# Kernel tuning notes

Measured on AMD Instinct MI355X. Metric: run time of the kernel, lower is better.

Reference implementation:

```python
import jax, jax.numpy as jnp
import numpy as np

B, E, H, LEVELS, MAXN = 16, 256, 256, 12, 2
N = 2 ** LEVELS - 1  # 4095 nodes, level-order perfect binary tree
NODE_VOCAB, EDGE_VOCAB = 64, 128

PARAM_SHAPES = {
    'node_emb': (NODE_VOCAB, E), 'edge_emb': (EDGE_VOCAB, E),
    'bu_Wioux': (E, 3 * H), 'bu_bioux': (3 * H,), 'bu_Wfx': (E, H), 'bu_bfx': (H,),
    'bu_Wiouh': (MAXN * H, 3 * H), 'bu_Wfh': (MAXN, MAXN * H, H),
    'bu_eWih': (E, 4 * H), 'bu_eWhh': (H, 4 * H), 'bu_ebih': (4 * H,), 'bu_ebhh': (4 * H,),
    'td_Wioux': (E, 3 * H), 'td_bioux': (3 * H,), 'td_Wfx': (E, H), 'td_bfx': (H,),
    'td_Wiouhc': (MAXN * H, 3 * H), 'td_Wiouhp': (H, 3 * H),
    'td_Wfchild': (MAXN, (MAXN + 1) * H, H), 'td_Wfparent': ((MAXN + 1) * H, H),
    'td_eWih': (E, 4 * H), 'td_eWhh': (H, 4 * H), 'td_ebih': (4 * H,), 'td_ebhh': (4 * H,),
}
FLOAT_NAMES = list(PARAM_SHAPES)

_sig = jax.nn.sigmoid

def _lstm(x, h, c, Wih, Whh, bih, bhh):
    # torch nn.LSTMCell gate order: i, f, g, o
    g = x @ Wih + h @ Whh + bih + bhh
    i, f, gg, o = jnp.split(g, 4, axis=-1)
    c2 = _sig(f) * c + _sig(i) * jnp.tanh(gg)
    return _sig(o) * jnp.tanh(c2), c2

def _forward(p, node_ids, edge_ids):
    x_all = p['node_emb'][node_ids]  # [B,N,E]
    e_all = p['edge_emb'][edge_ids]  # [B,N,E] edge to parent
    bu_h = [None] * LEVELS
    bu_he = [None] * LEVELS
    bu_ce = [None] * LEVELS
    # ---- bottom-up n-ary TreeLSTM, level by level (deepest first) ----
    for l in range(LEVELS - 1, -1, -1):
        M = 2 ** l
        s = M - 1
        x = x_all[:, s:s + M]
        if l == LEVELS - 1:  # leaves: zero-padded children (no fc terms)
            ch_h = jnp.zeros((B, M, MAXN, H), x.dtype)
            ch_c = ch_h
        else:
            ch_h = bu_he[l + 1].reshape(B, M, MAXN, H)
            ch_c = bu_ce[l + 1].reshape(B, M, MAXN, H)
        cat = ch_h.reshape(B, M, MAXN * H)  # child_cat_h
        iou = x @ p['bu_Wioux'] + p['bu_bioux'] + cat @ p['bu_Wiouh']
        i, o, u = jnp.split(iou, 3, axis=-1)
        i, o, u = _sig(i), _sig(o), jnp.tanh(u)
        fx = x @ p['bu_Wfx'] + p['bu_bfx']
        f = _sig(fx[:, :, None, :] + jnp.einsum('bmc,kch->bmkh', cat, p['bu_Wfh']))
        c = i * u + (f * ch_c).sum(axis=2)
        h = o * jnp.tanh(c)
        bu_h[l] = h
        # edge-transition LSTMCell before passing state to parent
        he, ce = _lstm(e_all[:, s:s + M], h, c, p['bu_eWih'], p['bu_eWhh'], p['bu_ebih'], p['bu_ebhh'])
        bu_he[l] = he
        bu_ce[l] = ce
    # ---- top-down n-ary TreeLSTM (root first) ----
    td_h = [None] * LEVELS
    ph = jnp.zeros((B, 1, H), x_all.dtype)
    pc = ph
    for l in range(LEVELS):
        M = 2 ** l
        s = M - 1
        x = x_all[:, s:s + M]
        if l == LEVELS - 1:
            ch_h = jnp.zeros((B, M, MAXN, H), x.dtype)
            ch_c = ch_h
        else:
            ch_h = bu_he[l + 1].reshape(B, M, MAXN, H)
            ch_c = bu_ce[l + 1].reshape(B, M, MAXN, H)
        cat = ch_h.reshape(B, M, MAXN * H)
        iou = x @ p['td_Wioux'] + p['td_bioux'] + cat @ p['td_Wiouhc'] + ph @ p['td_Wiouhp']
        i, o, u = jnp.split(iou, 3, axis=-1)
        i, o, u = _sig(i), _sig(o), jnp.tanh(u)
        fx = x @ p['td_Wfx'] + p['td_bfx']
        pcat = jnp.concatenate([ph, cat], axis=-1)  # [B,M,(MAXN+1)H]
        f_ch = _sig(fx[:, :, None, :] + jnp.einsum('bmc,kch->bmkh', pcat, p['td_Wfchild']))
        f_par = _sig(fx + pcat @ p['td_Wfparent'])
        c = i * u + (f_ch * ch_c).sum(axis=2) + f_par * pc
        h = o * jnp.tanh(c)
        td_h[l] = h
        if l < LEVELS - 1:
            M2 = 2 * M
            s2 = 2 * M - 1
            ph_r = jnp.repeat(h, 2, axis=1)
            pc_r = jnp.repeat(c, 2, axis=1)
            ph, pc = _lstm(e_all[:, s2:s2 + M2], ph_r, pc_r, p['td_eWih'], p['td_eWhh'], p['td_ebih'], p['td_ebhh'])
    return jnp.concatenate([jnp.concatenate(bu_h, 1), jnp.concatenate(td_h, 1)], axis=-1)  # [B,N,2H]


def setup_inputs() -> dict:
    key = jax.random.key(0)
    ks = jax.random.split(key, len(PARAM_SHAPES) + 2)
    inp = {}
    for k, (name, shp) in zip(ks, PARAM_SHAPES.items()):
        inp[name] = jax.random.normal(k, shp, dtype=jnp.float32) * 0.05
    inp['node_ids'] = jax.random.randint(ks[-2], (B, N), 0, NODE_VOCAB)
    inp['edge_ids'] = jax.random.randint(ks[-1], (B, N), 0, EDGE_VOCAB)
    return inp


def reference(node_emb, edge_emb, bu_Wioux, bu_bioux, bu_Wfx, bu_bfx, bu_Wiouh, bu_Wfh,
              bu_eWih, bu_eWhh, bu_ebih, bu_ebhh, td_Wioux, td_bioux, td_Wfx, td_bfx,
              td_Wiouhc, td_Wiouhp, td_Wfchild, td_Wfparent, td_eWih, td_eWhh, td_ebih, td_ebhh,
              node_ids, edge_ids):
    floats = (node_emb, edge_emb, bu_Wioux, bu_bioux, bu_Wfx, bu_bfx, bu_Wiouh, bu_Wfh,
              bu_eWih, bu_eWhh, bu_ebih, bu_ebhh, td_Wioux, td_bioux, td_Wfx, td_bfx,
              td_Wiouhc, td_Wiouhp, td_Wfchild, td_Wfparent, td_eWih, td_eWhh, td_ebih, td_ebhh)
    return _forward(dict(zip(FLOAT_NAMES, floats)), node_ids, edge_ids)
```

## Files before the change

### kernel.cpp

```cpp
#include <hip/hip_runtime.h>
#include <math.h>

#define NB 16
#define NH 256
#define NLV 12
#define NN 4095
#define OUTW 512

typedef unsigned short u16;
typedef unsigned int u32;
typedef __attribute__((ext_vector_type(4))) float f32x4;
typedef __attribute__((ext_vector_type(8))) short bf16x8;

__device__ __forceinline__ float sigf(float x){
  return __fdividef(1.0f, 1.0f + __expf(-x));
}
__device__ __forceinline__ float tanh_fast(float x){
  return 1.0f - __fdividef(2.0f, 1.0f + __expf(2.0f * x));
}

__device__ __forceinline__ u16 f2bf(float x){
  unsigned int u = __float_as_uint(x);
  return (u16)((u + 0x7fffu + ((u >> 16) & 1u)) >> 16);
}
__device__ __forceinline__ float bf2f(u16 h){
  return __uint_as_float(((unsigned int)h) << 16);
}

__device__ __forceinline__ void gload16(const void* g, void* l){
  __builtin_amdgcn_global_load_lds(
      (const __attribute__((address_space(1))) unsigned int*)g,
      (__attribute__((address_space(3))) unsigned int*)l, 16, 0, 0);
}

template<int VAR, int NG>
__global__ __launch_bounds__(256, 2) void fused_gemm(
    int R, int logM, int s,
    const int* __restrict__ ids,
    const u16* __restrict__ emb,
    const u16* __restrict__ hsrc,
    const u16* __restrict__ hsrc2,
    const u16* __restrict__ Wth, int wstride,
    const float* __restrict__ bias,
    const float* __restrict__ cce,
    const float* __restrict__ cprev,
    float* __restrict__ c_out,
    u16* __restrict__ h_out,
    float* __restrict__ out)
{
  constexpr int K0 = 256;
  constexpr int K1 = (VAR == 0) ? 512 : 256;
  constexpr int K2 = (VAR == 2 && NG == 6) ? 512 : 0;
  constexpr int KTOT = K0 + K1 + K2;
  constexpr int NSTEP = KTOT / 64;

  __shared__ u16 As[2][128][64];
  __shared__ u16 Bs[2][NG * 32][64];

  int bx = blockIdx.x;
  if ((gridDim.x & 7) == 0){
    int q = (int)gridDim.x >> 3;
    bx = (bx & 7) * q + (bx >> 3);
  }

  int tid = threadIdx.x, lane = tid & 63, w = tid >> 6;
  int wrow = w >> 1, whh = w & 1;
  int hh0 = blockIdx.y * 32;
  int M = 1 << logM;

  int lrow8 = lane >> 3;
  int gran  = lane & 7;
  int swz = (gran ^ lrow8) * 8;

  u32 off0[4]; u32 off1[4]; u32 off2[4];
  #pragma unroll
  for (int c = 0; c < 4; ++c){
    int gr = bx * 128 + c * 32 + w * 8 + lrow8;
    if (gr > R - 1) gr = R - 1;
    int b = gr >> logM, m = gr & (M - 1);
    int j = s + m;
    off0[c] = (u32)ids[b * NN + j] * 256u + (u32)swz;
    if constexpr (VAR == 0)
      off1[c] = (u32)(b * NN + 2 * j + 1) * (u32)NH + (u32)swz;
    else if constexpr (VAR == 3)
      off1[c] = (u32)(b * (M >> 1) + (m >> 1)) * (u32)NH + (u32)swz;
    else
      off1[c] = (u32)gr * (u32)NH + (u32)swz;
    if constexpr (K2 > 0)
      off2[c] = (u32)(b * NN + 2 * j + 1) * (u32)NH + (u32)swz;
    else
      off2[c] = 0;
  }
  u32 offB = (u32)(hh0 + w * 8 + lrow8) * (u32)wstride + (u32)swz;

  auto stage = [&](int buf, int kt){
    #pragma unroll
    for (int c = 0; c < 4; ++c){
      const u16* ga;
      if (kt < K0)               ga = emb   + off0[c] + kt;
      else if (kt < K0 + K1)     ga = hsrc  + off1[c] + (kt - K0);
      else                       ga = hsrc2 + off2[c] + (kt - K0 - K1);
      gload16(ga, &As[buf][c * 32 + w * 8][0]);
    }
    #pragma unroll
    for (int g = 0; g < NG; ++g)
      gload16(Wth + offB + (u32)(g * 256) * (u32)wstride + kt,
              &Bs[buf][g * 32 + w * 8][0]);
  };

  f32x4 acc[NG][4];
  #pragma unroll
  for (int g = 0; g < NG; ++g)
    #pragma unroll
    for (int i = 0; i < 4; ++i) acc[g][i] = (f32x4)0.0f;

  stage(0, 0);
  __syncthreads();

  #pragma unroll
  for (int st = 0; st < NSTEP; ++st){
    const int cur = st & 1;
    if (st + 1 < NSTEP) stage(cur ^ 1, (st + 1) * 64);

    #pragma unroll
    for (int kc = 0; kc < 2; ++kc){
      int g2 = ((kc * 4 + (lane >> 4)) ^ (lane & 7)) * 8;
      bf16x8 a[4];
      #pragma unroll
      for (int i = 0; i < 4; ++i)
        a[i] = *(const bf16x8*)&As[cur][wrow * 64 + i * 16 + (lane & 15)][g2];
      bf16x8 bf[NG];
      #pragma unroll
      for (int g = 0; g < NG; ++g)
        bf[g] = *(const bf16x8*)&Bs[cur][g * 32 + whh * 16 + (lane & 15)][g2];
      #pragma unroll
      for (int g = 0; g < NG; ++g)
        #pragma unroll
        for (int i = 0; i < 4; ++i)
          acc[g][i] = __builtin_amdgcn_mfma_f32_16x16x32_bf16(a[i], bf[g], acc[g][i], 0, 0, 0);
    }
    __syncthreads();
  }

  int hhL = hh0 + whh * 16 + (lane & 15);
  float bb[NG];
  #pragma unroll
  for (int g = 0; g < NG; ++g) bb[g] = bias[g * 256 + hhL];

  #pragma unroll
  for (int i = 0; i < 4; ++i){
    #pragma unroll
    for (int r = 0; r < 4; ++r){
      int row = bx * 128 + wrow * 64 + i * 16 + ((lane >> 4) << 2) + r;
      if (row >= R) continue;
      int b = row >> logM, m = row & (M - 1);
      int j = s + m;
      if constexpr (VAR == 0){
        float iv = sigf(acc[0][i][r] + bb[0]);
        float ov = sigf(acc[1][i][r] + bb[1]);
        float uv = tanh_fast(acc[2][i][r] + bb[2]);
        float c = iv * uv;
        float f0 = sigf(acc[3][i][r] + bb[3]);
        float f1 = sigf(acc[4 % NG][i][r] + bb[4 % NG]);
        c += f0 * cce[((size_t)(b * NN + 2 * j + 1)) * NH + hhL]
           + f1 * cce[((size_t)(b * NN + 2 * j + 2)) * NH + hhL];
        float h = ov * tanh_fast(c);
        c_out[(size_t)row * NH + hhL] = c;
        h_out[(size_t)row * NH + hhL] = f2bf(h);
        out[((size_t)(b * NN + j)) * OUTW + hhL] = h;
      } else if constexpr (VAR == 1){
        float iv = sigf(acc[0][i][r] + bb[0]);
        float fv = sigf(acc[1][i][r] + bb[1]);
        float gg = tanh_fast(acc[2][i][r] + bb[2]);
        float ov = sigf(acc[3 % NG][i][r] + bb[3 % NG]);
        float c2 = fv * cprev[(size_t)row * NH + hhL] + iv * gg;
        float h2 = ov * tanh_fast(c2);
        size_t di = ((size_t)(b * NN + j)) * NH + hhL;
        h_out[di] = f2bf(h2);
        c_out[di] = c2;
      } else if constexpr (VAR == 2){
        float iv = sigf(acc[0][i][r] + bb[0]);
        float ov = sigf(acc[1][i][r] + bb[1]);
        float uv = tanh_fast(acc[2][i][r] + bb[2]);
        float fp = sigf(acc[3 % NG][i][r] + bb[3 % NG]);
        float c = iv * uv + fp * cprev[(size_t)row * NH + hhL];
        if constexpr (NG == 6){
          float f0 = sigf(acc[4 % NG][i][r] + bb[4 % NG]);
          float f1 = sigf(acc[5 % NG][i][r] + bb[5 % NG]);
          c += f0 * cce[((size_t)(b * NN + 2 * j + 1)) * NH + hhL]
             + f1 * cce[((size_t)(b * NN + 2 * j + 2)) * NH + hhL];
        }
        float h = ov * tanh_fast(c);
        c_out[(size_t)row * NH + hhL] = c;
        h_out[(size_t)row * NH + hhL] = f2bf(h);
        out[((size_t)(b * NN + j)) * OUTW + NH + hhL] = h;
      } else {
        float iv = sigf(acc[0][i][r] + bb[0]);
        float fv = sigf(acc[1][i][r] + bb[1]);
        float gg = tanh_fast(acc[2][i][r] + bb[2]);
        float ov = sigf(acc[3 % NG][i][r] + bb[3 % NG]);
        int par = b * (M >> 1) + (m >> 1);
        float c2 = fv * cprev[(size_t)par * NH + hhL] + iv * gg;
        float h2 = ov * tanh_fast(c2);
        h_out[(size_t)row * NH + hhL] = f2bf(h2);
        c_out[(size_t)row * NH + hhL] = c2;
      }
    }
  }
}


__global__ void build_lut(int nids, int ncols, int stride,
                          const u16* __restrict__ embb,
                          const u16* __restrict__ Wt, int wstride,
                          const float* __restrict__ bias,
                          float* __restrict__ lut)
{
  int t = blockIdx.x * 256 + threadIdx.x;
  if (t >= nids * ncols) return;
  int id = t / ncols, n = t % ncols;
  const u16* e  = embb + id * 256;
  const u16* wv = Wt + (size_t)n * wstride;
  float z = bias[n];
  for (int k = 0; k < 256; k += 8){
    #pragma unroll
    for (int q = 0; q < 8; ++q)
      z += bf2f(e[k + q]) * bf2f(wv[k + q]);
  }
  int hh = n & 255, g = n >> 8;
  lut[((size_t)id * 256 + hh) * stride + g] = z;
}

__global__ void build_leaf(const float* __restrict__ lut64,
                           float* __restrict__ c64, float* __restrict__ h64f,
                           u16* __restrict__ h64b)
{
  int t = blockIdx.x * 256 + threadIdx.x;
  const float* lp = lut64 + (size_t)t * 3;
  float iv = sigf(lp[0]), ov = sigf(lp[1]), uv = tanh_fast(lp[2]);
  float c = iv * uv;
  float h = ov * tanh_fast(c);
  c64[t] = c; h64f[t] = h; h64b[t] = f2bf(h);
}

__global__ void leaf_gather(const int* __restrict__ node_ids,
                            const float* __restrict__ c64,
                            const float* __restrict__ h64f,
                            const u16* __restrict__ h64b,
                            float* __restrict__ c_lvl, u16* __restrict__ hl_b,
                            float* __restrict__ out)
{
  int t = blockIdx.x * 256 + threadIdx.x;
  int gr = t >> 6, q4 = (t & 63) << 2;
  int b = gr >> 11, m = gr & 2047;
  int j = 2047 + m;
  int id = node_ids[b * NN + j];
  float4 cv = *(const float4*)(c64 + id * 256 + q4);
  float4 hv = *(const float4*)(h64f + id * 256 + q4);
  uint2 hb  = *(const uint2*)(h64b + id * 256 + q4);
  *(float4*)(c_lvl + (size_t)gr * 256 + q4) = cv;
  *(uint2*)(hl_b + (size_t)gr * 256 + q4) = hb;
  *(float4*)(out + ((size_t)(b * NN + j)) * OUTW + q4) = hv;
}


__global__ void pack_bu_node_t(const float* __restrict__ Wioux, const float* __restrict__ Wiouh,
                               const float* __restrict__ Wfx, const float* __restrict__ Wfh,
                               const float* __restrict__ bioux, const float* __restrict__ bfx,
                               u16* __restrict__ Wth, float* __restrict__ bd)
{
  int tid = blockIdx.x*256 + threadIdx.x;
  if (tid < 768*1280){
    int n = tid / 768, k = tid % 768;
    float v;
    if (n < 768){
      v = (k < 256) ? Wioux[k*768 + n] : Wiouh[(k-256)*768 + n];
    } else {
      int kidx = (n < 1024) ? 0 : 1;
      int nn = n - 768 - kidx*256;
      v = (k < 256) ? Wfx[k*256 + nn] : Wfh[((size_t)kidx*512 + (k-256))*256 + nn];
    }
    Wth[tid] = f2bf(v);
  }
  if (tid < 1280) bd[tid] = (tid < 768) ? bioux[tid] : bfx[(tid-768) & 255];
}

__global__ void pack_edge_t(const float* __restrict__ Wih, const float* __restrict__ Whh,
                            const float* __restrict__ bih, const float* __restrict__ bhh,
                            u16* __restrict__ Wth, float* __restrict__ bd)
{
  int tid = blockIdx.x*256 + threadIdx.x;
  if (tid < 512*1024){
    int n = tid / 512, k = tid % 512;
    float v = (k < 256) ? Wih[k*1024 + n] : Whh[(k-256)*1024 + n];
    Wth[tid] = f2bf(v);
  }
  if (tid < 1024) bd[tid] = bih[tid] + bhh[tid];
}

__global__ void pack_td_node_t(const float* __restrict__ Wioux, const float* __restrict__ Wiouhc,
                               const float* __restrict__ Wiouhp, const float* __restrict__ Wfx,
                               const float* __restrict__ Wfchild, const float* __restrict__ Wfparent,
                               const float* __restrict__ bioux, const float* __restrict__ bfx,
                               u16* __restrict__ Wth, float* __restrict__ bd)
{
  int tid = blockIdx.x*256 + threadIdx.x;
  if (tid < 1024*1536){
    int n = tid / 1024, k = tid % 1024;
    float v;
    if (n < 768){
      v = (k < 256) ? Wioux[k*768 + n]
        : (k < 512) ? Wiouhp[(k-256)*768 + n]
                    : Wiouhc[(k-512)*768 + n];
    } else if (n < 1024){
      int nn = n - 768;
      v = (k < 256) ? Wfx[k*256 + nn] : Wfparent[(size_t)(k-256)*256 + nn];
    } else {
      int kidx = (n < 1280) ? 0 : 1;
      int nn = n - 1024 - kidx*256;
      v = (k < 256) ? Wfx[k*256 + nn]
                    : Wfchild[((size_t)kidx*768 + (k-256))*256 + nn];
    }
    Wth[tid] = f2bf(v);
  }
  if (tid < 1536) bd[tid] = (tid < 768) ? bioux[tid] : bfx[(tid-768) & 255];
}

__global__ void pack_emb(const float* __restrict__ ne, const float* __restrict__ ee,
                         u16* __restrict__ neb, u16* __restrict__ eeb,
                         u16* __restrict__ ph_b, float* __restrict__ pc)
{
  int tid = blockIdx.x*256 + threadIdx.x;
  if (tid < 64*256)  neb[tid] = f2bf(ne[tid]);
  if (tid < 128*256) eeb[tid] = f2bf(ee[tid]);
  if (tid < NB*NH){ ph_b[tid] = 0; pc[tid] = 0.0f; }
}

extern "C" void kernel_launch(void* const* d_in, const int* in_sizes, int n_in,
                              void* d_out, int out_size, void* d_ws, size_t ws_size,
                              hipStream_t stream)
{
  const float* node_emb  = (const float*)d_in[0];
  const float* edge_emb  = (const float*)d_in[1];
  const float* bu_Wioux  = (const float*)d_in[2];
  const float* bu_bioux  = (const float*)d_in[3];
  const float* bu_Wfx    = (const float*)d_in[4];
  const float* bu_bfx    = (const float*)d_in[5];
  const float* bu_Wiouh  = (const float*)d_in[6];
  const float* bu_Wfh    = (const float*)d_in[7];
  const float* bu_eWih   = (const float*)d_in[8];
  const float* bu_eWhh   = (const float*)d_in[9];
  const float* bu_ebih   = (const float*)d_in[10];
  const float* bu_ebhh   = (const float*)d_in[11];
  const float* td_Wioux  = (const float*)d_in[12];
  const float* td_bioux  = (const float*)d_in[13];
  const float* td_Wfx    = (const float*)d_in[14];
  const float* td_bfx    = (const float*)d_in[15];
  const float* td_Wiouhc = (const float*)d_in[16];
  const float* td_Wiouhp = (const float*)d_in[17];
  const float* td_Wfchild= (const float*)d_in[18];
  const float* td_Wfparent=(const float*)d_in[19];
  const float* td_eWih   = (const float*)d_in[20];
  const float* td_eWhh   = (const float*)d_in[21];
  const float* td_ebih   = (const float*)d_in[22];
  const float* td_ebhh   = (const float*)d_in[23];
  const int* node_ids    = (const int*)d_in[24];
  const int* edge_ids    = (const int*)d_in[25];
  float* out = (float*)d_out;

  float* fw = (float*)d_ws;
  size_t fo = 0;
  float* bbun = fw + fo; fo += 1280;
  float* bbue = fw + fo; fo += 1024;
  float* btdn = fw + fo; fo += 1536;
  float* btde = fw + fo; fo += 1024;
  float* lut64 = fw + fo; fo += (size_t)64*256*3;
  float* c64  = fw + fo; fo += (size_t)64*256;
  float* h64f = fw + fo; fo += (size_t)64*256;
  float* ce_all = fw + fo; fo += (size_t)NB*NN*NH;
  float* c_lvl  = fw + fo; fo += (size_t)NB*2048*NH;
  float* pc     = fw + fo; fo += (size_t)NB*2048*NH;

  u16* uw = (u16*)(fw + fo);
  size_t uo = 0;
  u16* Wbunh = uw + uo; uo += (size_t)768*1280;
  u16* Wbueh = uw + uo; uo += (size_t)512*1024;
  u16* Wtdnh = uw + uo; uo += (size_t)1024*1536;
  u16* Wtdeh = uw + uo; uo += (size_t)512*1024;
  u16* neb = uw + uo; uo += (size_t)64*256;
  u16* eeb = uw + uo; uo += (size_t)128*256;
  u16* h64b = uw + uo; uo += (size_t)64*256;
  u16* he_b = uw + uo; uo += (size_t)NB*NN*NH;
  u16* hl_b = uw + uo; uo += (size_t)NB*2048*NH;
  u16* ph_b = uw + uo; uo += (size_t)NB*2048*NH;

  pack_bu_node_t<<<(768*1280+255)/256, 256, 0, stream>>>(bu_Wioux, bu_Wiouh, bu_Wfx, bu_Wfh,
      bu_bioux, bu_bfx, Wbunh, bbun);
  pack_edge_t<<<(512*1024+255)/256, 256, 0, stream>>>(bu_eWih, bu_eWhh, bu_ebih, bu_ebhh,
      Wbueh, bbue);
  pack_td_node_t<<<(1024*1536+255)/256, 256, 0, stream>>>(td_Wioux, td_Wiouhc, td_Wiouhp, td_Wfx,
      td_Wfchild, td_Wfparent, td_bioux, td_bfx, Wtdnh, btdn);
  pack_edge_t<<<(512*1024+255)/256, 256, 0, stream>>>(td_eWih, td_eWhh, td_ebih, td_ebhh,
      Wtdeh, btde);
  pack_emb<<<(128*256+255)/256, 256, 0, stream>>>(node_emb, edge_emb, neb, eeb, ph_b, pc);

  build_lut<<<(64*768+255)/256, 256, 0, stream>>>(64, 768, 3, neb, Wbunh, 768, bbun, lut64);
  build_leaf<<<64, 256, 0, stream>>>(lut64, c64, h64f, h64b);

  {
    int R = NB * 2048;
    leaf_gather<<<(R * 64) / 256, 256, 0, stream>>>(node_ids, c64, h64f, h64b,
        c_lvl, hl_b, out);
    dim3 grid((R + 127) / 128, NH / 32);
    fused_gemm<1,4><<<grid, 256, 0, stream>>>(R, 11, 2047, edge_ids,
        eeb, hl_b, neb, Wbueh, 512, bbue,
        nullptr, c_lvl, ce_all, he_b, nullptr);
  }
  for (int l = NLV-2; l >= 0; --l){
    int M = 1<<l, s = M-1, R = NB*M;
    dim3 grid((R + 127) / 128, NH / 32);
    fused_gemm<0,5><<<grid, 256, 0, stream>>>(R, l, s, node_ids,
        neb, he_b, neb, Wbunh, 768, bbun,
        ce_all, nullptr, c_lvl, hl_b, out);
    if (l > 0){
      fused_gemm<1,4><<<grid, 256, 0, stream>>>(R, l, s, edge_ids,
          eeb, hl_b, neb, Wbueh, 512, bbue,
          nullptr, c_lvl, ce_all, he_b, nullptr);
    }
  }

  for (int l = 0; l < NLV; ++l){
    int M = 1<<l, s = M-1, R = NB*M;
    bool leaf = (l == NLV-1);
    dim3 grid((R + 127) / 128, NH / 32);
    if (!leaf){
      fused_gemm<2,6><<<grid, 256, 0, stream>>>(R, l, s, node_ids,
          neb, ph_b, he_b, Wtdnh, 1024, btdn,
          ce_all, pc, c_lvl, hl_b, out);
      int M2 = 2*M, s2 = 2*M-1, R2 = NB*M2;
      dim3 grid2((R2 + 127) / 128, NH / 32);
      fused_gemm<3,4><<<grid2, 256, 0, stream>>>(R2, l+1, s2, edge_ids,
          eeb, hl_b, neb, Wtdeh, 512, btde,
          nullptr, c_lvl, pc, ph_b, nullptr);
    } else {
      fused_gemm<2,4><<<grid, 256, 0, stream>>>(R, l, s, node_ids,
          neb, ph_b, neb, Wtdnh, 1024, btdn,
          nullptr, pc, c_lvl, hl_b, out);
    }
  }
}
```

Before: 1.169 ms.

## Replace leaf-level edge LSTM GEMM with vocabulary lookup tables

Leaf hidden state depends only on node id, and the edge input only on edge id. The change therefore precomputes per-id gate contributions (edge embedding × Wih and leaf h × Whh) into small LUTs and replaces the leaf-level edge LSTM GEMM over 32768 rows with a gather-and-add elementwise kernel. It also drops the leaf c/h level buffers that the GEMM needed. This removes the largest bottom-up GEMM at the cost of two small LUT-building launches, and the result relies on the leaves having zero children.

```diff
diff --git a/kernel.cpp b/kernel.cpp
--- a/kernel.cpp
+++ b/kernel.cpp
@@ -209,9 +209,8 @@
   }
 }
 
-
-__global__ void build_lut(int nids, int ncols, int stride,
-                          const u16* __restrict__ embb,
+__global__ void build_lut(int nids, int ncols, int stride, int koff,
+                          const u16* __restrict__ tab,
                           const u16* __restrict__ Wt, int wstride,
                           const float* __restrict__ bias,
                           float* __restrict__ lut)
@@ -219,9 +218,9 @@
   int t = blockIdx.x * 256 + threadIdx.x;
   if (t >= nids * ncols) return;
   int id = t / ncols, n = t % ncols;
-  const u16* e  = embb + id * 256;
-  const u16* wv = Wt + (size_t)n * wstride;
-  float z = bias[n];
+  const u16* e  = tab + id * 256;
+  const u16* wv = Wt + (size_t)n * wstride + koff;
+  float z = bias ? bias[n] : 0.0f;
   for (int k = 0; k < 256; k += 8){
     #pragma unroll
     for (int q = 0; q < 8; ++q)
@@ -244,10 +243,7 @@
 }
 
 __global__ void leaf_gather(const int* __restrict__ node_ids,
-                            const float* __restrict__ c64,
                             const float* __restrict__ h64f,
-                            const u16* __restrict__ h64b,
-                            float* __restrict__ c_lvl, u16* __restrict__ hl_b,
                             float* __restrict__ out)
 {
   int t = blockIdx.x * 256 + threadIdx.x;
@@ -255,12 +251,35 @@
   int b = gr >> 11, m = gr & 2047;
   int j = 2047 + m;
   int id = node_ids[b * NN + j];
-  float4 cv = *(const float4*)(c64 + id * 256 + q4);
   float4 hv = *(const float4*)(h64f + id * 256 + q4);
-  uint2 hb  = *(const uint2*)(h64b + id * 256 + q4);
-  *(float4*)(c_lvl + (size_t)gr * 256 + q4) = cv;
-  *(uint2*)(hl_b + (size_t)gr * 256 + q4) = hb;
   *(float4*)(out + ((size_t)(b * NN + j)) * OUTW + q4) = hv;
+}
+
+__global__ void leaf_edge(const int* __restrict__ node_ids,
+                          const int* __restrict__ edge_ids,
+                          const float* __restrict__ lutE,
+                          const float* __restrict__ lutH,
+                          const float* __restrict__ c64,
+                          u16* __restrict__ he_b, float* __restrict__ ce_all)
+{
+  int gr = blockIdx.x;
+  int hh = threadIdx.x;
+  int b = gr >> 11, m = gr & 2047;
+  int j = 2047 + m;
+  int nid = node_ids[b * NN + j];
+  int eid = edge_ids[b * NN + j];
+  float4 ge = *(const float4*)(lutE + ((size_t)eid * 256 + hh) * 4);
+  float4 gh = *(const float4*)(lutH + ((size_t)nid * 256 + hh) * 4);
+  float iv = sigf(ge.x + gh.x);
+  float fv = sigf(ge.y + gh.y);
+  float gg = tanh_fast(ge.z + gh.z);
+  float ov = sigf(ge.w + gh.w);
+  float cp = c64[nid * 256 + hh];
+  float c2 = fv * cp + iv * gg;
+  float h2 = ov * tanh_fast(c2);
+  size_t di = ((size_t)(b * NN + j)) * NH + hh;
+  he_b[di] = f2bf(h2);
+  ce_all[di] = c2;
 }
 
 
@@ -377,6 +396,8 @@
   float* lut64 = fw + fo; fo += (size_t)64*256*3;
   float* c64  = fw + fo; fo += (size_t)64*256;
   float* h64f = fw + fo; fo += (size_t)64*256;
+  float* lutE = fw + fo; fo += (size_t)128*256*4;
+  float* lutH = fw + fo; fo += (size_t)64*256*4;
   float* ce_all = fw + fo; fo += (size_t)NB*NN*NH;
   float* c_lvl  = fw + fo; fo += (size_t)NB*2048*NH;
   float* pc     = fw + fo; fo += (size_t)NB*2048*NH;
@@ -404,17 +425,15 @@
       Wtdeh, btde);
   pack_emb<<<(128*256+255)/256, 256, 0, stream>>>(node_emb, edge_emb, neb, eeb, ph_b, pc);
 
-  build_lut<<<(64*768+255)/256, 256, 0, stream>>>(64, 768, 3, neb, Wbunh, 768, bbun, lut64);
+  build_lut<<<(64*768+255)/256, 256, 0, stream>>>(64, 768, 3, 0, neb, Wbunh, 768, bbun, lut64);
   build_leaf<<<64, 256, 0, stream>>>(lut64, c64, h64f, h64b);
+  build_lut<<<(128*1024+255)/256, 256, 0, stream>>>(128, 1024, 4, 0,   eeb,  Wbueh, 512, bbue,  lutE);
+  build_lut<<<(64*1024+255)/256, 256, 0, stream>>>(64,  1024, 4, 256, h64b, Wbueh, 512, nullptr, lutH);
 
   {
     int R = NB * 2048;
-    leaf_gather<<<(R * 64) / 256, 256, 0, stream>>>(node_ids, c64, h64f, h64b,
-        c_lvl, hl_b, out);
-    dim3 grid((R + 127) / 128, NH / 32);
-    fused_gemm<1,4><<<grid, 256, 0, stream>>>(R, 11, 2047, edge_ids,
-        eeb, hl_b, neb, Wbueh, 512, bbue,
-        nullptr, c_lvl, ce_all, he_b, nullptr);
+    leaf_gather<<<(R * 64) / 256, 256, 0, stream>>>(node_ids, h64f, out);
+    leaf_edge<<<R, 256, 0, stream>>>(node_ids, edge_ids, lutE, lutH, c64, he_b, ce_all);
   }
   for (int l = NLV-2; l >= 0; --l){
     int M = 1<<l, s = M-1, R = NB*M;
```

Result: faster. 1.138 ms (-2.7%).
